# Performance work log

Hardware: AMD Instinct MI355X
Metric: run time of the kernel (lower is better)

The kernel has to match this reference:

```python
import jax, jax.numpy as jnp
import numpy as np

N_USERS = 200000
N_ITEMS = 100000
N_EDGES = 1000000
D = 64
NUM_LAYERS = 3
BATCH = 8192


def setup_inputs() -> dict:
    key = jax.random.key(0)
    ks = jax.random.split(key, 8)
    return {
        "user_feat": jax.random.normal(ks[0], (N_USERS, D), dtype=jnp.float32) * 0.1,
        "item_feat": jax.random.normal(ks[1], (N_ITEMS, D), dtype=jnp.float32) * 0.1,
        "edge_u": jax.random.randint(ks[2], (N_EDGES,), 0, N_USERS, dtype=jnp.int32),
        "edge_i": jax.random.randint(ks[3], (N_EDGES,), 0, N_ITEMS, dtype=jnp.int32),
        "norm": jax.random.uniform(ks[4], (N_EDGES,), dtype=jnp.float32),
        "users": jax.random.randint(ks[5], (BATCH,), 0, N_USERS, dtype=jnp.int32),
        "pos_items": jax.random.randint(ks[6], (BATCH,), 0, N_ITEMS, dtype=jnp.int32),
        "neg_items": jax.random.randint(ks[7], (BATCH,), 0, N_ITEMS, dtype=jnp.int32),
    }


def reference(user_feat, item_feat, edge_u, edge_i, norm, users, pos_items, neg_items):
    # LightGCN propagation: each layer does edge-weighted gather-scatter
    # (u_mul_e 'h','norm' -> sum) in both directions of the bipartite graph.
    u_h, i_h = user_feat, item_feat
    u_acc, i_acc = u_h, i_h
    w = norm[:, None]  # [E, 1]
    for _ in range(NUM_LAYERS):
        # user -> item messages
        new_i = jax.ops.segment_sum(u_h[edge_u] * w, edge_i, num_segments=N_ITEMS)
        # item -> user messages
        new_u = jax.ops.segment_sum(i_h[edge_i] * w, edge_u, num_segments=N_USERS)
        u_h, i_h = new_u, new_i
        u_acc = u_acc + u_h
        i_acc = i_acc + i_h
    scale = 1.0 / (NUM_LAYERS + 1)
    u_acc = u_acc * scale
    i_acc = i_acc * scale
    return (u_acc[users], i_acc[pos_items], i_acc[neg_items])
```

## Files before the change

### kernel.cpp

```cpp
#include <hip/hip_runtime.h>


#define N_USERS 200000
#define N_ITEMS 100000
#define N_EDGES 1000000
#define DIM 64
#define BATCH 8192
#define NTOT (N_USERS + N_ITEMS)
#define NOUT (3 * BATCH)
#define NPART 293
#define PLOCAL 1024
#define CAP 11264

#define HA 489
#define NUNITS (NTOT * DIM / 8)
#define OB (NOUT * 8 / 256)
#define AB8 (NTOT / 32)
#define PRB (NOUT / 1024)
#define PHB (NOUT * 8 / 1024)
#define CVB ((NUNITS + 4095) / 4096)
#define CPB ((NTOT / 4 + 1023) / 1024)

__device__ __forceinline__ unsigned f2bf(float f) {
    unsigned u = __float_as_uint(f);
    return (u + 0x7fffu + ((u >> 16) & 1u)) >> 16;
}
__device__ __forceinline__ uint2 pack4(float4 v) {
    uint2 o;
    o.x = f2bf(v.x) | (f2bf(v.y) << 16);
    o.y = f2bf(v.z) | (f2bf(v.w) << 16);
    return o;
}
__device__ __forceinline__ void fma4(float4& a, uint2 v, float w) {
    a.x += __uint_as_float(v.x << 16) * w;
    a.y += __uint_as_float(v.x & 0xffff0000u) * w;
    a.z += __uint_as_float(v.y << 16) * w;
    a.w += __uint_as_float(v.y & 0xffff0000u) * w;
}
__device__ __forceinline__ int out_bucket(int orow, const int* users,
                                          const int* pos, const int* neg) {
    int seg = orow >> 13;
    int b = orow & (BATCH - 1);
    if (seg == 0) return users[b];
    if (seg == 1) return N_USERS + pos[b];
    return N_USERS + neg[b];
}

__global__ void __launch_bounds__(1024)
prep_kernel(const int* __restrict__ users,
            const int* __restrict__ pos,
            const int* __restrict__ neg,
            const float* __restrict__ u_feat,
            const float* __restrict__ i_feat,
            unsigned char* __restrict__ isOut,
            int* __restrict__ flags,
            float* __restrict__ out)
{
    int bid = blockIdx.x, t = threadIdx.x;
    if (bid < PRB) {
        int orow = bid * 1024 + t;
        int bucket = out_bucket(orow, users, pos, neg);
        isOut[bucket] = 1;
        flags[bucket] = 1;
    } else {
        int idx = (bid - PRB) * 1024 + t;
        int row = idx >> 3;
        int d8 = (idx & 7) << 3;
        int seg = row >> 13;
        int b = row & (BATCH - 1);
        const float* src;
        if (seg == 0)      src = u_feat + (size_t)users[b] * DIM;
        else if (seg == 1) src = i_feat + (size_t)pos[b]   * DIM;
        else               src = i_feat + (size_t)neg[b]   * DIM;
        float4 v0 = *reinterpret_cast<const float4*>(src + d8);
        float4 v1 = *reinterpret_cast<const float4*>(src + d8 + 4);
        v0.x *= 0.25f; v0.y *= 0.25f; v0.z *= 0.25f; v0.w *= 0.25f;
        v1.x *= 0.25f; v1.y *= 0.25f; v1.z *= 0.25f; v1.w *= 0.25f;
        float* op = out + (size_t)row * DIM + d8;
        *reinterpret_cast<float4*>(op) = v0;
        *reinterpret_cast<float4*>(op + 4) = v1;
    }
}

__global__ void __launch_bounds__(256)
scatter_kernel(const int* __restrict__ eu,
               const int* __restrict__ ei,
               const float* __restrict__ w,
               int* __restrict__ gcur,
               uint2* __restrict__ partBuf,
               const unsigned char* __restrict__ isOut,
               int* __restrict__ flags)
{
    __shared__ int lh[NPART];
    __shared__ int lcur[NPART];
    int bid = blockIdx.x, t = threadIdx.x;
    for (int k = t; k < NPART; k += 256) lh[k] = 0;
    __syncthreads();
    int e0 = (bid * 256 + t) * 8;
    bool act = e0 < N_EDGES;
    int4 u0, u1, i0, i1;
    if (act) {
        u0 = *reinterpret_cast<const int4*>(eu + e0);
        u1 = *reinterpret_cast<const int4*>(eu + e0 + 4);
        i0 = *reinterpret_cast<const int4*>(ei + e0);
        i1 = *reinterpret_cast<const int4*>(ei + e0 + 4);
        atomicAdd(&lh[u0.x >> 10], 1);
        atomicAdd(&lh[u0.y >> 10], 1);
        atomicAdd(&lh[u0.z >> 10], 1);
        atomicAdd(&lh[u0.w >> 10], 1);
        atomicAdd(&lh[u1.x >> 10], 1);
        atomicAdd(&lh[u1.y >> 10], 1);
        atomicAdd(&lh[u1.z >> 10], 1);
        atomicAdd(&lh[u1.w >> 10], 1);
        atomicAdd(&lh[(N_USERS + i0.x) >> 10], 1);
        atomicAdd(&lh[(N_USERS + i0.y) >> 10], 1);
        atomicAdd(&lh[(N_USERS + i0.z) >> 10], 1);
        atomicAdd(&lh[(N_USERS + i0.w) >> 10], 1);
        atomicAdd(&lh[(N_USERS + i1.x) >> 10], 1);
        atomicAdd(&lh[(N_USERS + i1.y) >> 10], 1);
        atomicAdd(&lh[(N_USERS + i1.z) >> 10], 1);
        atomicAdd(&lh[(N_USERS + i1.w) >> 10], 1);
    }
    __syncthreads();
    for (int k = t; k < NPART; k += 256) {
        int v = lh[k];
        lcur[k] = v ? atomicAdd(&gcur[k], v) : 0;
    }
    __syncthreads();
    if (act) {
        float4 wa = *reinterpret_cast<const float4*>(w + e0);
        float4 wb = *reinterpret_cast<const float4*>(w + e0 + 4);
        int us[8] = {u0.x, u0.y, u0.z, u0.w, u1.x, u1.y, u1.z, u1.w};
        int is[8] = {i0.x, i0.y, i0.z, i0.w, i1.x, i1.y, i1.z, i1.w};
        float ws[8] = {wa.x, wa.y, wa.z, wa.w, wb.x, wb.y, wb.z, wb.w};
        #pragma unroll
        for (int j = 0; j < 8; ++j) {
            int bu = us[j];
            int bi = N_USERS + is[j];
            unsigned wbits = __float_as_uint(ws[j]);
            int pu = bu >> 10, pi = bi >> 10;
            int su = atomicAdd(&lcur[pu], 1);
            partBuf[(size_t)pu * CAP + su] =
                make_uint2((unsigned)(bu & 1023) | ((unsigned)bi << 10), wbits);
            int si = atomicAdd(&lcur[pi], 1);
            partBuf[(size_t)pi * CAP + si] =
                make_uint2((unsigned)(bi & 1023) | ((unsigned)bu << 10), wbits);
            if (isOut[bu]) flags[bi] = 1;
            if (isOut[bi]) flags[bu] = 1;
        }
    }
}

__global__ void __launch_bounds__(1024)
mid_kernel(const int* __restrict__ gcur,
           const uint2* __restrict__ partBuf,
           int2* __restrict__ rp2,
           int2* __restrict__ entries,
           const float4* __restrict__ uf4,
           const float4* __restrict__ if4,
           unsigned short* __restrict__ F0,
           const int* __restrict__ flags,
           int* __restrict__ list,
           int* __restrict__ count)
{
    int bid = blockIdx.x, t = threadIdx.x;
    if (bid < NPART) {
        __shared__ int h[PLOCAL];
        __shared__ int cur[PLOCAL];
        __shared__ int wsum[16];
        int p = bid;
        int base = p * CAP;
        int end = base + gcur[p];
        h[t] = 0;
        __syncthreads();
        for (int r = base + t; r < end; r += 1024)
            atomicAdd(&h[partBuf[r].x & 1023], 1);
        __syncthreads();
        int v = h[t];
        int s = v;
        #pragma unroll
        for (int off = 1; off < 64; off <<= 1) {
            int x = __shfl_up(s, off, 64);
            if ((t & 63) >= off) s += x;
        }
        if ((t & 63) == 63) wsum[t >> 6] = s;
        __syncthreads();
        if (t < 16) {
            int ws = wsum[t];
            int acc = ws;
            #pragma unroll
            for (int off = 1; off < 16; off <<= 1) {
                int x = __shfl_up(acc, off, 64);
                if (t >= off) acc += x;
            }
            wsum[t] = acc - ws;
        }
        __syncthreads();
        int excl = (s - v) + wsum[t >> 6];
        int c0 = base + excl;
        cur[t] = c0;
        int gb = p * PLOCAL + t;
        if (gb < NTOT) rp2[gb] = make_int2(c0, v);
        __syncthreads();
        for (int r = base + t; r < end; r += 1024) {
            uint2 rec = partBuf[r];
            int slot = atomicAdd(&cur[rec.x & 1023], 1);
            entries[slot] = make_int2((int)(rec.x >> 10), (int)rec.y);
        }
    } else if (bid < NPART + CVB) {
        const int NU4 = N_USERS * DIM / 4;
        int jb = (bid - NPART) * 4096 + t;
        float4 a[4], b[4];
        #pragma unroll
        for (int c = 0; c < 4; ++c) {
            int j = jb + c * 1024;
            if (j < NUNITS) {
                int f4 = j * 2;
                if (f4 < NU4) { a[c] = uf4[f4];       b[c] = uf4[f4 + 1]; }
                else          { a[c] = if4[f4 - NU4]; b[c] = if4[f4 - NU4 + 1]; }
            }
        }
        #pragma unroll
        for (int c = 0; c < 4; ++c) {
            int j = jb + c * 1024;
            if (j < NUNITS) {
                uint2 pa = pack4(a[c]), pb = pack4(b[c]);
                *reinterpret_cast<uint4*>(F0 + (size_t)j * 8) =
                    make_uint4(pa.x, pa.y, pb.x, pb.y);
            }
        }
    } else {
        int idx = ((bid - NPART - CVB) * 1024 + t) * 4;
        if (idx >= NTOT) return;
        int4 f = *reinterpret_cast<const int4*>(flags + idx);
        int loc[4]; int k = 0;
        if (f.x) loc[k++] = idx;
        if (f.y) loc[k++] = idx + 1;
        if (f.z) loc[k++] = idx + 2;
        if (f.w) loc[k++] = idx + 3;
        if (k) {
            int base = atomicAdd(count, k);
            for (int m = 0; m < k; ++m) list[base + m] = loc[m];
        }
    }
}

__device__ __forceinline__ void agg_row8(int2 rc, int l8, int gb,
                                         const int2* __restrict__ entries,
                                         const unsigned short* __restrict__ src,
                                         float4& sL, float4& sH)
{
    int beg = rc.x, cnt = rc.y;
    float4 a0L = {0,0,0,0}, a0H = {0,0,0,0}, a1L = {0,0,0,0}, a1H = {0,0,0,0};
    for (int base = 0; base < cnt; base += 8) {
        int2 e = make_int2(0, 0);
        if (base + l8 < cnt) e = entries[beg + base + l8];
        int   c[8];
        float wv[8];
        #pragma unroll
        for (int k = 0; k < 8; ++k) {
            c[k]  = __shfl(e.x, gb + k);
            wv[k] = __int_as_float(__shfl(e.y, gb + k));
        }
        uint4 v[8];
        #pragma unroll
        for (int k = 0; k < 8; ++k)
            v[k] = *reinterpret_cast<const uint4*>(
                src + (size_t)c[k] * DIM + l8 * 8);
        #pragma unroll
        for (int k = 0; k < 8; ++k) {
            if (k & 1) {
                fma4(a1L, make_uint2(v[k].x, v[k].y), wv[k]);
                fma4(a1H, make_uint2(v[k].z, v[k].w), wv[k]);
            } else {
                fma4(a0L, make_uint2(v[k].x, v[k].y), wv[k]);
                fma4(a0H, make_uint2(v[k].z, v[k].w), wv[k]);
            }
        }
    }
    sL.x = a0L.x + a1L.x; sL.y = a0L.y + a1L.y;
    sL.z = a0L.z + a1L.z; sL.w = a0L.w + a1L.w;
    sH.x = a0H.x + a1H.x; sH.y = a0H.y + a1H.y;
    sH.z = a0H.z + a1H.z; sH.w = a0H.w + a1H.w;
}

__global__ void agg1_kernel(const int2* __restrict__ rp2,
                            const int2* __restrict__ entries,
                            const unsigned short* __restrict__ F0,
                            unsigned short* __restrict__ H1)
{
    int gid = blockIdx.x * 256 + threadIdx.x;
    int lane = gid & 63;
    int l8 = lane & 7;
    int gb = lane & 56;
    int row = gid >> 3;
    if (row >= NTOT) return;
    float4 sL, sH;
    agg_row8(rp2[row], l8, gb, entries, F0, sL, sH);
    uint2 pL = pack4(sL), pH = pack4(sH);
    *reinterpret_cast<uint4*>(H1 + (size_t)row * DIM + l8 * 8) =
        make_uint4(pL.x, pL.y, pH.x, pH.y);
}

__global__ void agg2_add1_kernel(const int2* __restrict__ rp2,
                                 const int2* __restrict__ entries,
                                 const unsigned short* __restrict__ H1,
                                 unsigned short* __restrict__ H2,
                                 const int* __restrict__ list,
                                 const int* __restrict__ count,
                                 const int* __restrict__ users,
                                 const int* __restrict__ pos,
                                 const int* __restrict__ neg,
                                 float* __restrict__ out)
{
    int bid = blockIdx.x;
    if (bid < AB8) {
        int gid = bid * 256 + threadIdx.x;
        int lane = gid & 63;
        int l8 = lane & 7;
        int gb = lane & 56;
        int idx = gid >> 3;
        int n = *count;
        if (idx >= n) return;
        int row = list[idx];
        float4 sL, sH;
        agg_row8(rp2[row], l8, gb, entries, H1, sL, sH);
        uint2 pL = pack4(sL), pH = pack4(sH);
        *reinterpret_cast<uint4*>(H2 + (size_t)row * DIM + l8 * 8) =
            make_uint4(pL.x, pL.y, pH.x, pH.y);
    } else {
        int idx = (bid - AB8) * 256 + threadIdx.x;
        int row = idx >> 3;
        if (row >= NOUT) return;
        int d8 = (idx & 7) << 3;
        int bucket = out_bucket(row, users, pos, neg);
        uint4 v = *reinterpret_cast<const uint4*>(H1 + (size_t)bucket * DIM + d8);
        float* op = out + (size_t)row * DIM + d8;
        float4 o0 = *reinterpret_cast<const float4*>(op);
        float4 o1 = *reinterpret_cast<const float4*>(op + 4);
        o0.x += 0.25f * __uint_as_float(v.x << 16);
        o0.y += 0.25f * __uint_as_float(v.x & 0xffff0000u);
        o0.z += 0.25f * __uint_as_float(v.y << 16);
        o0.w += 0.25f * __uint_as_float(v.y & 0xffff0000u);
        o1.x += 0.25f * __uint_as_float(v.z << 16);
        o1.y += 0.25f * __uint_as_float(v.z & 0xffff0000u);
        o1.z += 0.25f * __uint_as_float(v.w << 16);
        o1.w += 0.25f * __uint_as_float(v.w & 0xffff0000u);
        *reinterpret_cast<float4*>(op) = o0;
        *reinterpret_cast<float4*>(op + 4) = o1;
    }
}

__global__ void aggout_add2_kernel(const int2* __restrict__ rp2,
                                   const int2* __restrict__ entries,
                                   const unsigned short* __restrict__ H2,
                                   const int* __restrict__ users,
                                   const int* __restrict__ pos,
                                   const int* __restrict__ neg,
                                   float* __restrict__ out)
{
    int gid = blockIdx.x * 256 + threadIdx.x;
    int lane = gid & 63;
    int l8 = lane & 7;
    int gb = lane & 56;
    int orow = gid >> 3;
    if (orow >= NOUT) return;
    int bucket = out_bucket(orow, users, pos, neg);
    float4 sL, sH;
    agg_row8(rp2[bucket], l8, gb, entries, H2, sL, sH);
    uint4 v = *reinterpret_cast<const uint4*>(H2 + (size_t)bucket * DIM + l8 * 8);
    sL.x += __uint_as_float(v.x << 16);
    sL.y += __uint_as_float(v.x & 0xffff0000u);
    sL.z += __uint_as_float(v.y << 16);
    sL.w += __uint_as_float(v.y & 0xffff0000u);
    sH.x += __uint_as_float(v.z << 16);
    sH.y += __uint_as_float(v.z & 0xffff0000u);
    sH.z += __uint_as_float(v.w << 16);
    sH.w += __uint_as_float(v.w & 0xffff0000u);
    float* op = out + (size_t)orow * DIM + l8 * 8;
    float4 o0 = *reinterpret_cast<const float4*>(op);
    float4 o1 = *reinterpret_cast<const float4*>(op + 4);
    o0.x += 0.25f * sL.x; o0.y += 0.25f * sL.y;
    o0.z += 0.25f * sL.z; o0.w += 0.25f * sL.w;
    o1.x += 0.25f * sH.x; o1.y += 0.25f * sH.y;
    o1.z += 0.25f * sH.z; o1.w += 0.25f * sH.w;
    *reinterpret_cast<float4*>(op) = o0;
    *reinterpret_cast<float4*>(op + 4) = o1;
}

extern "C" void kernel_launch(void* const* d_in, const int* in_sizes, int n_in,
                              void* d_out, int out_size, void* d_ws, size_t ws_size,
                              hipStream_t stream)
{
    const float* user_feat = (const float*)d_in[0];
    const float* item_feat = (const float*)d_in[1];
    const int*   eu        = (const int*)d_in[2];
    const int*   ei        = (const int*)d_in[3];
    const float* norm      = (const float*)d_in[4];
    const int*   users     = (const int*)d_in[5];
    const int*   pos       = (const int*)d_in[6];
    const int*   neg       = (const int*)d_in[7];
    float* out = (float*)d_out;

    auto align256 = [](size_t x) { return (x + 255) & ~(size_t)255; };
    const size_t hBytes = (size_t)NTOT * DIM * sizeof(unsigned short);
    const size_t pBytes = (size_t)NPART * CAP * 8;

    char* p = (char*)d_ws;
    unsigned short* F0 = (unsigned short*)p; p += align256(hBytes);
    unsigned short* H1 = (unsigned short*)p; p += align256(hBytes);
    unsigned short* H2 = (unsigned short*)p; p += align256(hBytes);
    const size_t zBytes = (size_t)(512 + NTOT + 16) * 4 + NTOT;
    int* gcur = (int*)p;
    int* flags = gcur + 512;
    int* count = flags + NTOT;
    unsigned char* isOut = (unsigned char*)(count + 16);
    p += align256(zBytes);
    int2* rp2      = (int2*)p;  p += align256((size_t)NTOT * 8);
    uint2* partBuf = (uint2*)p; p += align256(pBytes);
    int*  list     = (int*)p;   p += align256((size_t)NTOT * 4);
    int2* entries  = (int2*)p;  p += align256(pBytes);

    hipMemsetAsync(gcur, 0, zBytes, stream);

    prep_kernel<<<PRB + PHB, 1024, 0, stream>>>(
        users, pos, neg, user_feat, item_feat, isOut, flags, out);

    scatter_kernel<<<HA, 256, 0, stream>>>(
        eu, ei, norm, gcur, partBuf, isOut, flags);

    mid_kernel<<<NPART + CVB + CPB, 1024, 0, stream>>>(
        gcur, partBuf, rp2, entries,
        (const float4*)user_feat, (const float4*)item_feat, F0,
        flags, list, count);

    agg1_kernel<<<AB8, 256, 0, stream>>>(rp2, entries, F0, H1);

    agg2_add1_kernel<<<AB8 + OB, 256, 0, stream>>>(
        rp2, entries, H1, H2, list, count, users, pos, neg, out);

    aggout_add2_kernel<<<NOUT / 32, 256, 0, stream>>>(
        rp2, entries, H2, users, pos, neg, out);
}
```

Baseline: 268.3 us.

## Compute layer-2 frontier flags from CSR after build, drop prep kernel and compaction list

```diff
diff --git a/kernel.cpp b/kernel.cpp
--- a/kernel.cpp
+++ b/kernel.cpp
@@ -16,10 +16,10 @@
 #define NUNITS (NTOT * DIM / 8)
 #define OB (NOUT * 8 / 256)
 #define AB8 (NTOT / 32)
-#define PRB (NOUT / 1024)
-#define PHB (NOUT * 8 / 1024)
+#define FB ((NOUT + 255) / 256)
 #define CVB ((NUNITS + 4095) / 4096)
-#define CPB ((NTOT / 4 + 1023) / 1024)
+#define HB0 (NOUT * 8 / 1024)
+#define ZFB ((NTOT / 4 + 1023) / 1024)
 
 __device__ __forceinline__ unsigned f2bf(float f) {
     unsigned u = __float_as_uint(f);
@@ -46,50 +46,12 @@
     return N_USERS + neg[b];
 }
 
-__global__ void __launch_bounds__(1024)
-prep_kernel(const int* __restrict__ users,
-            const int* __restrict__ pos,
-            const int* __restrict__ neg,
-            const float* __restrict__ u_feat,
-            const float* __restrict__ i_feat,
-            unsigned char* __restrict__ isOut,
-            int* __restrict__ flags,
-            float* __restrict__ out)
-{
-    int bid = blockIdx.x, t = threadIdx.x;
-    if (bid < PRB) {
-        int orow = bid * 1024 + t;
-        int bucket = out_bucket(orow, users, pos, neg);
-        isOut[bucket] = 1;
-        flags[bucket] = 1;
-    } else {
-        int idx = (bid - PRB) * 1024 + t;
-        int row = idx >> 3;
-        int d8 = (idx & 7) << 3;
-        int seg = row >> 13;
-        int b = row & (BATCH - 1);
-        const float* src;
-        if (seg == 0)      src = u_feat + (size_t)users[b] * DIM;
-        else if (seg == 1) src = i_feat + (size_t)pos[b]   * DIM;
-        else               src = i_feat + (size_t)neg[b]   * DIM;
-        float4 v0 = *reinterpret_cast<const float4*>(src + d8);
-        float4 v1 = *reinterpret_cast<const float4*>(src + d8 + 4);
-        v0.x *= 0.25f; v0.y *= 0.25f; v0.z *= 0.25f; v0.w *= 0.25f;
-        v1.x *= 0.25f; v1.y *= 0.25f; v1.z *= 0.25f; v1.w *= 0.25f;
-        float* op = out + (size_t)row * DIM + d8;
-        *reinterpret_cast<float4*>(op) = v0;
-        *reinterpret_cast<float4*>(op + 4) = v1;
-    }
-}
-
 __global__ void __launch_bounds__(256)
 scatter_kernel(const int* __restrict__ eu,
                const int* __restrict__ ei,
                const float* __restrict__ w,
                int* __restrict__ gcur,
-               uint2* __restrict__ partBuf,
-               const unsigned char* __restrict__ isOut,
-               int* __restrict__ flags)
+               uint2* __restrict__ partBuf)
 {
     __shared__ int lh[NPART];
     __shared__ int lcur[NPART];
@@ -145,8 +107,6 @@
             int si = atomicAdd(&lcur[pi], 1);
             partBuf[(size_t)pi * CAP + si] =
                 make_uint2((unsigned)(bi & 1023) | ((unsigned)bu << 10), wbits);
-            if (isOut[bu]) flags[bi] = 1;
-            if (isOut[bi]) flags[bu] = 1;
         }
     }
 }
@@ -159,9 +119,13 @@
            const float4* __restrict__ uf4,
            const float4* __restrict__ if4,
            unsigned short* __restrict__ F0,
-           const int* __restrict__ flags,
-           int* __restrict__ list,
-           int* __restrict__ count)
+           const float* __restrict__ u_feat,
+           const float* __restrict__ i_feat,
+           const int* __restrict__ users,
+           const int* __restrict__ pos,
+           const int* __restrict__ neg,
+           float* __restrict__ out,
+           int* __restrict__ flags)
 {
     int bid = blockIdx.x, t = threadIdx.x;
     if (bid < NPART) {
@@ -229,19 +193,27 @@
                     make_uint4(pa.x, pa.y, pb.x, pb.y);
             }
         }
+    } else if (bid < NPART + CVB + HB0) {
+        int idx = (bid - NPART - CVB) * 1024 + t;
+        int row = idx >> 3;
+        int d8 = (idx & 7) << 3;
+        int seg = row >> 13;
+        int b = row & (BATCH - 1);
+        const float* src;
+        if (seg == 0)      src = u_feat + (size_t)users[b] * DIM;
+        else if (seg == 1) src = i_feat + (size_t)pos[b]   * DIM;
+        else               src = i_feat + (size_t)neg[b]   * DIM;
+        float4 v0 = *reinterpret_cast<const float4*>(src + d8);
+        float4 v1 = *reinterpret_cast<const float4*>(src + d8 + 4);
+        v0.x *= 0.25f; v0.y *= 0.25f; v0.z *= 0.25f; v0.w *= 0.25f;
+        v1.x *= 0.25f; v1.y *= 0.25f; v1.z *= 0.25f; v1.w *= 0.25f;
+        float* op = out + (size_t)row * DIM + d8;
+        *reinterpret_cast<float4*>(op) = v0;
+        *reinterpret_cast<float4*>(op + 4) = v1;
     } else {
-        int idx = ((bid - NPART - CVB) * 1024 + t) * 4;
-        if (idx >= NTOT) return;
-        int4 f = *reinterpret_cast<const int4*>(flags + idx);
-        int loc[4]; int k = 0;
-        if (f.x) loc[k++] = idx;
-        if (f.y) loc[k++] = idx + 1;
-        if (f.z) loc[k++] = idx + 2;
-        if (f.w) loc[k++] = idx + 3;
-        if (k) {
-            int base = atomicAdd(count, k);
-            for (int m = 0; m < k; ++m) list[base + m] = loc[m];
-        }
+        int i4 = (bid - NPART - CVB - HB0) * 1024 + t;
+        if (i4 < NTOT / 4)
+            reinterpret_cast<int4*>(flags)[i4] = make_int4(0, 0, 0, 0);
     }
 }
 
@@ -284,34 +256,14 @@
     sH.z = a0H.z + a1H.z; sH.w = a0H.w + a1H.w;
 }
 
-__global__ void agg1_kernel(const int2* __restrict__ rp2,
-                            const int2* __restrict__ entries,
-                            const unsigned short* __restrict__ F0,
-                            unsigned short* __restrict__ H1)
-{
-    int gid = blockIdx.x * 256 + threadIdx.x;
-    int lane = gid & 63;
-    int l8 = lane & 7;
-    int gb = lane & 56;
-    int row = gid >> 3;
-    if (row >= NTOT) return;
-    float4 sL, sH;
-    agg_row8(rp2[row], l8, gb, entries, F0, sL, sH);
-    uint2 pL = pack4(sL), pH = pack4(sH);
-    *reinterpret_cast<uint4*>(H1 + (size_t)row * DIM + l8 * 8) =
-        make_uint4(pL.x, pL.y, pH.x, pH.y);
-}
-
-__global__ void agg2_add1_kernel(const int2* __restrict__ rp2,
+__global__ void agg1_flag_kernel(const int2* __restrict__ rp2,
                                  const int2* __restrict__ entries,
-                                 const unsigned short* __restrict__ H1,
-                                 unsigned short* __restrict__ H2,
-                                 const int* __restrict__ list,
-                                 const int* __restrict__ count,
+                                 const unsigned short* __restrict__ F0,
+                                 unsigned short* __restrict__ H1,
                                  const int* __restrict__ users,
                                  const int* __restrict__ pos,
                                  const int* __restrict__ neg,
-                                 float* __restrict__ out)
+                                 int* __restrict__ flags)
 {
     int bid = blockIdx.x;
     if (bid < AB8) {
@@ -319,10 +271,43 @@
         int lane = gid & 63;
         int l8 = lane & 7;
         int gb = lane & 56;
-        int idx = gid >> 3;
-        int n = *count;
-        if (idx >= n) return;
-        int row = list[idx];
+        int row = gid >> 3;
+        if (row >= NTOT) return;
+        float4 sL, sH;
+        agg_row8(rp2[row], l8, gb, entries, F0, sL, sH);
+        uint2 pL = pack4(sL), pH = pack4(sH);
+        *reinterpret_cast<uint4*>(H1 + (size_t)row * DIM + l8 * 8) =
+            make_uint4(pL.x, pL.y, pH.x, pH.y);
+    } else {
+        int t = (bid - AB8) * 256 + threadIdx.x;
+        if (t >= NOUT) return;
+        int bucket = out_bucket(t, users, pos, neg);
+        flags[bucket] = 1;
+        int2 rc = rp2[bucket];
+        for (int k = rc.x; k < rc.x + rc.y; ++k)
+            flags[entries[k].x] = 1;
+    }
+}
+
+__global__ void agg2_add1_kernel(const int2* __restrict__ rp2,
+                                 const int2* __restrict__ entries,
+                                 const unsigned short* __restrict__ H1,
+                                 unsigned short* __restrict__ H2,
+                                 const int* __restrict__ flags,
+                                 const int* __restrict__ users,
+                                 const int* __restrict__ pos,
+                                 const int* __restrict__ neg,
+                                 float* __restrict__ out)
+{
+    int bid = blockIdx.x;
+    if (bid < AB8) {
+        int gid = bid * 256 + threadIdx.x;
+        int lane = gid & 63;
+        int l8 = lane & 7;
+        int gb = lane & 56;
+        int row = gid >> 3;
+        if (row >= NTOT) return;
+        if (!flags[row]) return;
         float4 sL, sH;
         agg_row8(rp2[row], l8, gb, entries, H1, sL, sH);
         uint2 pL = pack4(sL), pH = pack4(sH);
@@ -410,34 +395,26 @@
     unsigned short* F0 = (unsigned short*)p; p += align256(hBytes);
     unsigned short* H1 = (unsigned short*)p; p += align256(hBytes);
     unsigned short* H2 = (unsigned short*)p; p += align256(hBytes);
-    const size_t zBytes = (size_t)(512 + NTOT + 16) * 4 + NTOT;
-    int* gcur = (int*)p;
-    int* flags = gcur + 512;
-    int* count = flags + NTOT;
-    unsigned char* isOut = (unsigned char*)(count + 16);
-    p += align256(zBytes);
+    int* gcur  = (int*)p;       p += align256(512 * 4);
+    int* flags = (int*)p;       p += align256((size_t)NTOT * 4);
     int2* rp2      = (int2*)p;  p += align256((size_t)NTOT * 8);
     uint2* partBuf = (uint2*)p; p += align256(pBytes);
-    int*  list     = (int*)p;   p += align256((size_t)NTOT * 4);
     int2* entries  = (int2*)p;  p += align256(pBytes);
 
-    hipMemsetAsync(gcur, 0, zBytes, stream);
-
-    prep_kernel<<<PRB + PHB, 1024, 0, stream>>>(
-        users, pos, neg, user_feat, item_feat, isOut, flags, out);
-
-    scatter_kernel<<<HA, 256, 0, stream>>>(
-        eu, ei, norm, gcur, partBuf, isOut, flags);
-
-    mid_kernel<<<NPART + CVB + CPB, 1024, 0, stream>>>(
+    hipMemsetAsync(gcur, 0, 512 * 4, stream);
+
+    scatter_kernel<<<HA, 256, 0, stream>>>(eu, ei, norm, gcur, partBuf);
+
+    mid_kernel<<<NPART + CVB + HB0 + ZFB, 1024, 0, stream>>>(
         gcur, partBuf, rp2, entries,
         (const float4*)user_feat, (const float4*)item_feat, F0,
-        flags, list, count);
-
-    agg1_kernel<<<AB8, 256, 0, stream>>>(rp2, entries, F0, H1);
+        user_feat, item_feat, users, pos, neg, out, flags);
+
+    agg1_flag_kernel<<<AB8 + FB, 256, 0, stream>>>(
+        rp2, entries, F0, H1, users, pos, neg, flags);
 
     agg2_add1_kernel<<<AB8 + OB, 256, 0, stream>>>(
-        rp2, entries, H1, H2, list, count, users, pos, neg, out);
+        rp2, entries, H1, H2, flags, users, pos, neg, out);
 
     aggout_add2_kernel<<<NOUT / 32, 256, 0, stream>>>(
         rp2, entries, H2, users, pos, neg, out);
```

New measurement: 260.9 us. -2.8%, faster.
